# Kernel tuning notes

Hardware: AMD Instinct MI355X
Metric: run time of the kernel (lower is better)

## Reference

```python
import jax, jax.numpy as jnp
import numpy as np

B, S, D, H = 2, 2048, 1024, 16
DK = D // H


def setup_inputs() -> dict:
    key = jax.random.key(0)
    ks = jax.random.split(key, 11)
    scale = 1.0 / np.sqrt(D)
    inp = {
        "q": jax.random.normal(ks[0], (B, S, D), jnp.float32),
        "k": jax.random.normal(ks[1], (B, S, D), jnp.float32),
        "v": jax.random.normal(ks[2], (B, S, D), jnp.float32),
        # causal mask, broadcastable to (B, H, S, S); 0 = masked
        "mask": jnp.tril(jnp.ones((S, S), jnp.int32))[None, None, :, :],
        "wq": jax.random.normal(ks[3], (D, D), jnp.float32) * scale,
        "bq": jax.random.normal(ks[4], (D,), jnp.float32) * scale,
        "wk": jax.random.normal(ks[5], (D, D), jnp.float32) * scale,
        "bk": jax.random.normal(ks[6], (D,), jnp.float32) * scale,
        "wv": jax.random.normal(ks[7], (D, D), jnp.float32) * scale,
        "bv": jax.random.normal(ks[8], (D,), jnp.float32) * scale,
        "wo": jax.random.normal(ks[9], (D, D), jnp.float32) * scale,
        "bo": jax.random.normal(ks[10], (D,), jnp.float32) * scale,
    }
    return inp


def reference(q, k, v, mask, wq, bq, wk, bk, wv, bv, wo, bo):
    # Linear projections (torch Linear: y = x @ W^T + b)
    Q = jnp.einsum('bsd,ed->bse', q, wq) + bq
    K = jnp.einsum('bsd,ed->bse', k, wk) + bk
    V = jnp.einsum('bsd,ed->bse', v, wv) + bv
    # split heads -> (B, H, S, d_k)
    Q = Q.reshape(B, S, H, DK).transpose(0, 2, 1, 3)
    K = K.reshape(B, S, H, DK).transpose(0, 2, 1, 3)
    V = V.reshape(B, S, H, DK).transpose(0, 2, 1, 3)
    # naive full-score attention, faithful to the source
    scores = jnp.einsum('bhqd,bhkd->bhqk', Q, K) / jnp.sqrt(jnp.float32(DK))
    scores = jnp.where(mask == 0, -jnp.inf, scores)
    attn = jax.nn.softmax(scores, axis=-1)
    out = jnp.einsum('bhqk,bhkd->bhqd', attn, V)
    # merge heads -> (B, S, D)
    out = out.transpose(0, 2, 1, 3).reshape(B, S, D)
    return jnp.einsum('bsd,ed->bse', out, wo) + bo
```

## Files before the change

kernel.cpp:

```cpp
#include <hip/hip_runtime.h>
#include <hip/hip_bf16.h>
#include <cstdint>

constexpr int Bc = 2, Sc = 2048, Dc = 1024, Hc = 16;
constexpr int Mtok = Bc * Sc;

typedef __bf16 bf16;
typedef __bf16 bf16x4 __attribute__((ext_vector_type(4)));
typedef __bf16 bf16x8 __attribute__((ext_vector_type(8)));
typedef float  f32x4  __attribute__((ext_vector_type(4)));

__device__ __forceinline__ void gld_lds16(const bf16* g, bf16* l) {
  __builtin_amdgcn_global_load_lds(
      (__attribute__((address_space(1))) void*)(void*)g,
      (__attribute__((address_space(3))) void*)l, 16, 0, 0);
}

__global__ __launch_bounds__(256) void convert_all(
    const float* __restrict__ q, const float* __restrict__ k,
    const float* __restrict__ v, const float* __restrict__ wq,
    const float* __restrict__ wk, const float* __restrict__ wv,
    const float* __restrict__ wo, bf16* __restrict__ ws)
{
  constexpr size_t NQ = (size_t)Mtok * Dc;
  constexpr size_t NW = (size_t)Dc * Dc;
  const size_t e = ((size_t)blockIdx.x * 256 + threadIdx.x) * 8;
  const float* src; bf16* dst;
  if (e < 3 * NQ) {
    src = (e < NQ) ? q + e : (e < 2 * NQ) ? k + (e - NQ) : v + (e - 2 * NQ);
    dst = ws + e;
  } else {
    const size_t w = e - 3 * NQ;
    const float* wsrc = (w < NW) ? wq : (w < 2 * NW) ? wk : (w < 3 * NW) ? wv : wo;
    src = wsrc + (w & (NW - 1));
    dst = ws + 5 * NQ + w;
  }
  f32x4 a = ((const f32x4*)src)[0];
  f32x4 b = ((const f32x4*)src)[1];
  bf16x8 t;
  t[0]=(bf16)a[0]; t[1]=(bf16)a[1]; t[2]=(bf16)a[2]; t[3]=(bf16)a[3];
  t[4]=(bf16)b[0]; t[5]=(bf16)b[1]; t[6]=(bf16)b[2]; t[7]=(bf16)b[3];
  *(bf16x8*)dst = t;
}

__global__ __launch_bounds__(256) void gemm_qkv(
    const bf16* __restrict__ Aq, const bf16* __restrict__ Ak,
    const bf16* __restrict__ Av, const bf16* __restrict__ Wb,
    const float* __restrict__ bq, const float* __restrict__ bk,
    const float* __restrict__ bv,
    bf16* __restrict__ Yq, bf16* __restrict__ Yk, bf16* __restrict__ Vt)
{
  __shared__ __attribute__((aligned(16))) bf16 As[128 * 64];
  __shared__ __attribute__((aligned(16))) bf16 Bs[128 * 64];

  const int z = blockIdx.z;
  const bf16*  A    = (z == 0) ? Aq : (z == 1) ? Ak : Av;
  const bf16*  Wz   = Wb + (size_t)z * Dc * Dc;
  const float* bias = (z == 0) ? bq : (z == 1) ? bk : bv;

  const int m0 = blockIdx.x * 128, n0 = blockIdx.y * 128;
  const int tid = threadIdx.x, wave = tid >> 6, lane = tid & 63;
  const int quad = lane >> 4, l16 = lane & 15;
  const int rw = wave >> 1, cw = wave & 1;
  const int swz = l16 & 7;
  const int srow = wave * 8 + (lane >> 3);
  const int scol = ((lane & 7) ^ (lane >> 3)) * 8;

  f32x4 acc[4][4] = {};

  for (int k0 = 0; k0 < Dc; k0 += 64) {
#pragma unroll
    for (int s = 0; s < 4; ++s) {
      gld_lds16(A  + (size_t)(m0 + s * 32 + srow) * Dc + k0 + scol,
                &As[(s * 32 + wave * 8) * 64]);
      gld_lds16(Wz + (size_t)(n0 + s * 32 + srow) * Dc + k0 + scol,
                &Bs[(s * 32 + wave * 8) * 64]);
    }
    __syncthreads();
#pragma unroll
    for (int ks = 0; ks < 2; ++ks) {
      bf16x8 af[4];
#pragma unroll
      for (int rt = 0; rt < 4; ++rt)
        af[rt] = *(const bf16x8*)
            &As[(rw * 64 + rt * 16 + l16) * 64 + (((ks * 4 + quad) ^ swz) * 8)];
#pragma unroll
      for (int ct = 0; ct < 4; ++ct) {
        bf16x8 bfr = *(const bf16x8*)
            &Bs[(cw * 64 + ct * 16 + l16) * 64 + (((ks * 4 + quad) ^ swz) * 8)];
#pragma unroll
        for (int rt = 0; rt < 4; ++rt)
          acc[rt][ct] = __builtin_amdgcn_mfma_f32_16x16x32_bf16(af[rt], bfr, acc[rt][ct], 0, 0, 0);
      }
    }
    __syncthreads();
  }

  if (z < 2) {
    bf16* Y = (z == 0) ? Yq : Yk;
#pragma unroll
    for (int ct = 0; ct < 4; ++ct) {
      const int col = n0 + cw * 64 + ct * 16 + l16;
      const float bvv = bias[col];
#pragma unroll
      for (int rt = 0; rt < 4; ++rt)
#pragma unroll
        for (int i = 0; i < 4; ++i) {
          const int row = m0 + rw * 64 + rt * 16 + quad * 4 + i;
          Y[(size_t)row * Dc + col] = (bf16)(acc[rt][ct][i] + bvv);
        }
    }
  } else {
#pragma unroll
    for (int ct = 0; ct < 4; ++ct) {
      const int col = n0 + cw * 64 + ct * 16 + l16;
      const float bvv = bias[col];
#pragma unroll
      for (int rt = 0; rt < 4; ++rt) {
        const int row0 = m0 + rw * 64 + rt * 16 + quad * 4;
        const int bb = row0 >> 11, s0 = row0 & 2047;
        bf16x4 pk;
#pragma unroll
        for (int i = 0; i < 4; ++i) pk[i] = (bf16)(acc[rt][ct][i] + bvv);
        *(bf16x4*)&Vt[((size_t)bb * Dc + col) * Sc + s0] = pk;
      }
    }
  }
}

__global__ __launch_bounds__(256) void gemm_o(
    const bf16* __restrict__ A, const bf16* __restrict__ Wz,
    const float* __restrict__ bias, float* __restrict__ Y)
{
  __shared__ __attribute__((aligned(16))) bf16 As[128 * 64];
  __shared__ __attribute__((aligned(16))) bf16 Bs[128 * 64];

  const int m0 = blockIdx.x * 128, n0 = blockIdx.y * 128;
  const int tid = threadIdx.x, wave = tid >> 6, lane = tid & 63;
  const int quad = lane >> 4, l16 = lane & 15;
  const int rw = wave >> 1, cw = wave & 1;
  const int swz = l16 & 7;
  const int srow = wave * 8 + (lane >> 3);
  const int scol = ((lane & 7) ^ (lane >> 3)) * 8;

  f32x4 acc[4][4] = {};

  for (int k0 = 0; k0 < Dc; k0 += 64) {
#pragma unroll
    for (int s = 0; s < 4; ++s) {
      gld_lds16(A  + (size_t)(m0 + s * 32 + srow) * Dc + k0 + scol,
                &As[(s * 32 + wave * 8) * 64]);
      gld_lds16(Wz + (size_t)(n0 + s * 32 + srow) * Dc + k0 + scol,
                &Bs[(s * 32 + wave * 8) * 64]);
    }
    __syncthreads();
#pragma unroll
    for (int ks = 0; ks < 2; ++ks) {
      bf16x8 af[4];
#pragma unroll
      for (int rt = 0; rt < 4; ++rt)
        af[rt] = *(const bf16x8*)
            &As[(rw * 64 + rt * 16 + l16) * 64 + (((ks * 4 + quad) ^ swz) * 8)];
#pragma unroll
      for (int ct = 0; ct < 4; ++ct) {
        bf16x8 bfr = *(const bf16x8*)
            &Bs[(cw * 64 + ct * 16 + l16) * 64 + (((ks * 4 + quad) ^ swz) * 8)];
#pragma unroll
        for (int rt = 0; rt < 4; ++rt)
          acc[rt][ct] = __builtin_amdgcn_mfma_f32_16x16x32_bf16(af[rt], bfr, acc[rt][ct], 0, 0, 0);
      }
    }
    __syncthreads();
  }

#pragma unroll
  for (int ct = 0; ct < 4; ++ct) {
    const int col = n0 + cw * 64 + ct * 16 + l16;
    const float bvv = bias[col];
#pragma unroll
    for (int rt = 0; rt < 4; ++rt)
#pragma unroll
      for (int i = 0; i < 4; ++i) {
        const int row = m0 + rw * 64 + rt * 16 + quad * 4 + i;
        Y[(size_t)row * Dc + col] = acc[rt][ct][i] + bvv;
      }
  }
}

template <bool AF32, bool BF32, bool OUTF32>
__global__ __launch_bounds__(256) void gemm128(
    const void* __restrict__ Av, const void* __restrict__ Bv,
    const float* __restrict__ bias, void* __restrict__ Yv,
    int M, int N, int K)
{
  __shared__ __attribute__((aligned(16))) bf16 As[2][128][40];
  __shared__ __attribute__((aligned(16))) bf16 Bs[2][128][40];

  const int m0 = blockIdx.x * 128, n0 = blockIdx.y * 128;
  const int tid = threadIdx.x, wave = tid >> 6, lane = tid & 63;
  const int quad = lane >> 4, l16 = lane & 15;
  const int rw = wave >> 1, cw = wave & 1;
  const int srow = tid >> 1, sc = (tid & 1) * 16;

  f32x4 acc[4][4] = {};

  auto load = [&](const void* P, bool f32, int r0, int k0, bf16x8& lo, bf16x8& hi) {
    if (f32) {
      const float* s = (const float*)P + (size_t)(r0 + srow) * K + k0 + sc;
      f32x4 a0 = ((const f32x4*)s)[0], a1 = ((const f32x4*)s)[1];
      f32x4 a2 = ((const f32x4*)s)[2], a3 = ((const f32x4*)s)[3];
      lo[0]=(bf16)a0[0]; lo[1]=(bf16)a0[1]; lo[2]=(bf16)a0[2]; lo[3]=(bf16)a0[3];
      lo[4]=(bf16)a1[0]; lo[5]=(bf16)a1[1]; lo[6]=(bf16)a1[2]; lo[7]=(bf16)a1[3];
      hi[0]=(bf16)a2[0]; hi[1]=(bf16)a2[1]; hi[2]=(bf16)a2[2]; hi[3]=(bf16)a2[3];
      hi[4]=(bf16)a3[0]; hi[5]=(bf16)a3[1]; hi[6]=(bf16)a3[2]; hi[7]=(bf16)a3[3];
    } else {
      const bf16* s = (const bf16*)P + (size_t)(r0 + srow) * K + k0 + sc;
      lo = ((const bf16x8*)s)[0]; hi = ((const bf16x8*)s)[1];
    }
  };

  bf16x8 alo, ahi, blo, bhi;
  load(Av, AF32, m0, 0, alo, ahi); load(Bv, BF32, n0, 0, blo, bhi);
  *(bf16x8*)&As[0][srow][sc] = alo; *(bf16x8*)&As[0][srow][sc + 8] = ahi;
  *(bf16x8*)&Bs[0][srow][sc] = blo; *(bf16x8*)&Bs[0][srow][sc + 8] = bhi;

  const int NIT = K >> 5;
  for (int it = 0; it < NIT; ++it) {
    __syncthreads();
    const int cur = it & 1;
    const bool pf = (it + 1) < NIT;
    if (pf) { load(Av, AF32, m0, (it+1)*32, alo, ahi); load(Bv, BF32, n0, (it+1)*32, blo, bhi); }

    bf16x8 af[4];
#pragma unroll
    for (int rt = 0; rt < 4; ++rt)
      af[rt] = *(const bf16x8*)&As[cur][rw * 64 + rt * 16 + l16][quad * 8];
#pragma unroll
    for (int ct = 0; ct < 4; ++ct) {
      bf16x8 bfr = *(const bf16x8*)&Bs[cur][cw * 64 + ct * 16 + l16][quad * 8];
#pragma unroll
      for (int rt = 0; rt < 4; ++rt)
        acc[rt][ct] = __builtin_amdgcn_mfma_f32_16x16x32_bf16(af[rt], bfr, acc[rt][ct], 0, 0, 0);
    }
    if (pf) {
      const int nxt = cur ^ 1;
      *(bf16x8*)&As[nxt][srow][sc] = alo; *(bf16x8*)&As[nxt][srow][sc + 8] = ahi;
      *(bf16x8*)&Bs[nxt][srow][sc] = blo; *(bf16x8*)&Bs[nxt][srow][sc + 8] = bhi;
    }
  }

#pragma unroll
  for (int ct = 0; ct < 4; ++ct) {
    const int col = n0 + cw * 64 + ct * 16 + l16;
    const float bvv = bias[col];
#pragma unroll
    for (int rt = 0; rt < 4; ++rt)
#pragma unroll
      for (int i = 0; i < 4; ++i) {
        const int row = m0 + rw * 64 + rt * 16 + quad * 4 + i;
        const float vv = acc[rt][ct][i] + bvv;
        if constexpr (OUTF32) ((float*)Yv)[(size_t)row * N + col] = vv;
        else                  ((bf16*)Yv)[(size_t)row * N + col] = (bf16)vv;
      }
  }
}

__global__ __launch_bounds__(256) void transpose_v(
    const bf16* __restrict__ in, bf16* __restrict__ out)
{
  __shared__ __attribute__((aligned(16))) bf16 tile[64][72];
  const int s0 = blockIdx.x * 64, d0 = blockIdx.y * 64, b = blockIdx.z;
  const int t = threadIdx.x, r = t >> 2, c = (t & 3) * 16;

  const bf16* src = in + (size_t)(b * Sc + s0 + r) * Dc + d0 + c;
  *(bf16x8*)&tile[r][c]     = ((const bf16x8*)src)[0];
  *(bf16x8*)&tile[r][c + 8] = ((const bf16x8*)src)[1];
  __syncthreads();

  bf16x8 t0, t1;
#pragma unroll
  for (int j = 0; j < 8; ++j) t0[j] = tile[c + j][r];
#pragma unroll
  for (int j = 0; j < 8; ++j) t1[j] = tile[c + 8 + j][r];
  bf16* dst = out + (size_t)(b * Dc + d0 + r) * Sc + s0 + c;
  ((bf16x8*)dst)[0] = t0;
  ((bf16x8*)dst)[1] = t1;
}

__global__ __launch_bounds__(256, 6) void attn5(
    const bf16* __restrict__ Q, const bf16* __restrict__ K,
    const bf16* __restrict__ Vt, bf16* __restrict__ O)
{
  __shared__ __attribute__((aligned(16))) bf16 Ks[64 * 64];
  __shared__ __attribute__((aligned(16))) bf16 Vs[64 * 64];
  __shared__ __attribute__((aligned(16))) bf16 Ps[4][16][68];

  const int bh = blockIdx.x, b = bh >> 4, h = bh & 15;
  const int qy = blockIdx.y;
  const int qt = (qy & 8) ? ((qy & 24) | (7 - (qy & 7))) : qy;
  const int q0 = qt * 64;
  const int nkb = qt + 1;

  const int tid = threadIdx.x, wave = tid >> 6, lane = tid & 63;
  const int quad = lane >> 4, l16 = lane & 15;
  const int swz = l16 & 7;
  const int sr  = lane >> 3;
  const int sgc = ((lane & 7) ^ sr) * 8;

  const bf16 onec = (bf16)1.0f;
  const bf16x8 ones = {onec, onec, onec, onec, onec, onec, onec, onec};

  const bf16* qrow = Q + (size_t)(b * Sc + q0 + wave * 16 + l16) * Dc + h * 64 + quad * 8;
  const bf16x8 aq0 = *(const bf16x8*)qrow;
  const bf16x8 aq1 = *(const bf16x8*)(qrow + 32);

  f32x4 oacc[4] = {{0,0,0,0},{0,0,0,0},{0,0,0,0},{0,0,0,0}};
  f32x4 lacc = {0, 0, 0, 0};

  for (int kb = 0; kb < nkb; ++kb) {
    __syncthreads();
#pragma unroll
    for (int j = 0; j < 2; ++j) {
      const int r = wave * 16 + j * 8 + sr;
      gld_lds16(K  + (size_t)(b * Sc + kb * 64 + r) * Dc + h * 64 + sgc,
                &Ks[(wave * 16 + j * 8) * 64]);
      gld_lds16(Vt + (size_t)(b * Dc + h * 64 + r) * Sc + kb * 64 + sgc,
                &Vs[(wave * 16 + j * 8) * 64]);
    }
    __syncthreads();

    f32x4 s[4] = {{0,0,0,0},{0,0,0,0},{0,0,0,0},{0,0,0,0}};
#pragma unroll
    for (int d2 = 0; d2 < 2; ++d2) {
      const bf16x8 bq = d2 ? aq1 : aq0;
#pragma unroll
      for (int ct = 0; ct < 4; ++ct) {
        bf16x8 ak = *(const bf16x8*)
            &Ks[(ct * 16 + l16) * 64 + (((d2 * 4 + quad) ^ swz) * 8)];
        s[ct] = __builtin_amdgcn_mfma_f32_16x16x32_bf16(ak, bq, s[ct], 0, 0, 0);
      }
    }

    if (kb == nkb - 1) {
      const int qcol = wave * 16 + l16;
#pragma unroll
      for (int ct = 0; ct < 4; ++ct) {
        const int key0 = ct * 16 + quad * 4;
        bf16x4 pk;
#pragma unroll
        for (int i = 0; i < 4; ++i)
          pk[i] = (bf16)((key0 + i > qcol) ? 0.f : __expf(s[ct][i] * 0.125f));
        *(bf16x4*)&Ps[wave][l16][key0] = pk;
      }
    } else {
#pragma unroll
      for (int ct = 0; ct < 4; ++ct) {
        bf16x4 pk;
#pragma unroll
        for (int i = 0; i < 4; ++i) pk[i] = (bf16)__expf(s[ct][i] * 0.125f);
        *(bf16x4*)&Ps[wave][l16][ct * 16 + quad * 4] = pk;
      }
    }

    const bf16x8 ap0 = *(const bf16x8*)&Ps[wave][l16][quad * 8];
    const bf16x8 ap1 = *(const bf16x8*)&Ps[wave][l16][32 + quad * 8];

    lacc = __builtin_amdgcn_mfma_f32_16x16x32_bf16(ap0, ones, lacc, 0, 0, 0);
    lacc = __builtin_amdgcn_mfma_f32_16x16x32_bf16(ap1, ones, lacc, 0, 0, 0);

#pragma unroll
    for (int d2 = 0; d2 < 2; ++d2) {
      const bf16x8 ap = d2 ? ap1 : ap0;
#pragma unroll
      for (int ct = 0; ct < 4; ++ct) {
        bf16x8 bv = *(const bf16x8*)
            &Vs[(ct * 16 + l16) * 64 + (((d2 * 4 + quad) ^ swz) * 8)];
        oacc[ct] = __builtin_amdgcn_mfma_f32_16x16x32_bf16(ap, bv, oacc[ct], 0, 0, 0);
      }
    }
  }

  f32x4 rl;
#pragma unroll
  for (int i = 0; i < 4; ++i) rl[i] = 1.0f / lacc[i];
#pragma unroll
  for (int ct = 0; ct < 4; ++ct)
#pragma unroll
    for (int i = 0; i < 4; ++i)
      O[(size_t)(b * Sc + q0 + wave * 16 + quad * 4 + i) * Dc + h * 64 + ct * 16 + l16] =
          (bf16)(oacc[ct][i] * rl[i]);
}

extern "C" void kernel_launch(void* const* d_in, const int* in_sizes, int n_in,
                              void* d_out, int out_size, void* d_ws, size_t ws_size,
                              hipStream_t stream)
{
  const float* q  = (const float*)d_in[0];
  const float* k  = (const float*)d_in[1];
  const float* v  = (const float*)d_in[2];
  const float* wq = (const float*)d_in[4];
  const float* bq = (const float*)d_in[5];
  const float* wk = (const float*)d_in[6];
  const float* bk = (const float*)d_in[7];
  const float* wv = (const float*)d_in[8];
  const float* bv = (const float*)d_in[9];
  const float* wo = (const float*)d_in[10];
  const float* bo = (const float*)d_in[11];
  float* out = (float*)d_out;

  constexpr size_t NQ = (size_t)Mtok * Dc;
  constexpr size_t NW = (size_t)Dc * Dc;
  bf16* W = (bf16*)d_ws;
  const dim3 ga(Hc * Bc, 32);
  const dim3 gt(Sc / 64, Dc / 64, Bc);

  const bool fancy = ws_size >= (size_t)(6 * NQ + 4 * NW) * 2;
  if (fancy) {
    bf16* xq = W;
    bf16* xk = W + NQ;
    bf16* xv = W + 2 * NQ;
    bf16* Qp = W + 3 * NQ;
    bf16* Kp = W + 4 * NQ;
    bf16* wb = W + 5 * NQ;
    bf16* Vt = W + 5 * NQ + 4 * NW;
    bf16* AO = W;

    convert_all<<<8192, 256, 0, stream>>>(q, k, v, wq, wk, wv, wo, W);
    gemm_qkv<<<dim3(Mtok / 128, Dc / 128, 3), 256, 0, stream>>>(
        xq, xk, xv, wb, bq, bk, bv, Qp, Kp, Vt);
    attn5<<<ga, 256, 0, stream>>>(Qp, Kp, Vt, AO);
    gemm_o<<<dim3(Mtok / 128, Dc / 128), 256, 0, stream>>>(AO, wb + 3 * NW, bo, out);
  } else {
    bf16* Qp = W;
    bf16* Kp = W + NQ;
    bf16* Vp = W + 2 * NQ;
    bf16* Vt = W + 3 * NQ;
    bf16* AO = W + 4 * NQ;
    const dim3 gg(Mtok / 128, Dc / 128);
    gemm128<true, true, false><<<gg, 256, 0, stream>>>(q, wq, bq, Qp, Mtok, Dc, Dc);
    gemm128<true, true, false><<<gg, 256, 0, stream>>>(k, wk, bk, Kp, Mtok, Dc, Dc);
    gemm128<true, true, false><<<gg, 256, 0, stream>>>(v, wv, bv, Vp, Mtok, Dc, Dc);
    transpose_v<<<gt, 256, 0, stream>>>(Vp, Vt);
    attn5<<<ga, 256, 0, stream>>>(Qp, Kp, Vt, AO);
    gemm128<false, true, true><<<gg, 256, 0, stream>>>(AO, wo, bo, out, Mtok, Dc, Dc);
  }
}
```

Before: 228.5 us.

## Fuse fp32-to-bf16 conversion into GEMM tile staging, drop convert kernel

Removes the separate convert_all kernel that wrote bf16 copies of q/k/v and all weights to workspace. The QKV and output GEMMs now load fp32 tiles directly through registers, convert to bf16 and write them into swizzled LDS, which saves a full read-write pass over the inputs and one launch. The cost is that these staging loads go through registers instead of direct global-to-LDS loads, and each fp32 weight/activation tile is converted repeatedly by every block that reads it. The workspace requirement also drops.

```diff
diff --git a/kernel.cpp b/kernel.cpp
--- a/kernel.cpp
+++ b/kernel.cpp
@@ -16,36 +16,28 @@
       (__attribute__((address_space(3))) void*)l, 16, 0, 0);
 }
 
-__global__ __launch_bounds__(256) void convert_all(
+__device__ __forceinline__ void stage_f32_128x64(
+    const float* __restrict__ g, int ldg, bf16* __restrict__ lds, int tid)
+{
+  const int sc  = tid & 7;
+  const int sr0 = tid >> 3;
+  const int lc  = (sc ^ (sr0 & 7)) * 8;
+#pragma unroll
+  for (int j = 0; j < 4; ++j) {
+    const int r = sr0 + 32 * j;
+    const float* s = g + (size_t)r * ldg + lc;
+    f32x4 a = ((const f32x4*)s)[0], b = ((const f32x4*)s)[1];
+    bf16x8 t;
+    t[0]=(bf16)a[0]; t[1]=(bf16)a[1]; t[2]=(bf16)a[2]; t[3]=(bf16)a[3];
+    t[4]=(bf16)b[0]; t[5]=(bf16)b[1]; t[6]=(bf16)b[2]; t[7]=(bf16)b[3];
+    *(bf16x8*)&lds[r * 64 + sc * 8] = t;
+  }
+}
+
+__global__ __launch_bounds__(256) void gemm_qkv(
     const float* __restrict__ q, const float* __restrict__ k,
     const float* __restrict__ v, const float* __restrict__ wq,
     const float* __restrict__ wk, const float* __restrict__ wv,
-    const float* __restrict__ wo, bf16* __restrict__ ws)
-{
-  constexpr size_t NQ = (size_t)Mtok * Dc;
-  constexpr size_t NW = (size_t)Dc * Dc;
-  const size_t e = ((size_t)blockIdx.x * 256 + threadIdx.x) * 8;
-  const float* src; bf16* dst;
-  if (e < 3 * NQ) {
-    src = (e < NQ) ? q + e : (e < 2 * NQ) ? k + (e - NQ) : v + (e - 2 * NQ);
-    dst = ws + e;
-  } else {
-    const size_t w = e - 3 * NQ;
-    const float* wsrc = (w < NW) ? wq : (w < 2 * NW) ? wk : (w < 3 * NW) ? wv : wo;
-    src = wsrc + (w & (NW - 1));
-    dst = ws + 5 * NQ + w;
-  }
-  f32x4 a = ((const f32x4*)src)[0];
-  f32x4 b = ((const f32x4*)src)[1];
-  bf16x8 t;
-  t[0]=(bf16)a[0]; t[1]=(bf16)a[1]; t[2]=(bf16)a[2]; t[3]=(bf16)a[3];
-  t[4]=(bf16)b[0]; t[5]=(bf16)b[1]; t[6]=(bf16)b[2]; t[7]=(bf16)b[3];
-  *(bf16x8*)dst = t;
-}
-
-__global__ __launch_bounds__(256) void gemm_qkv(
-    const bf16* __restrict__ Aq, const bf16* __restrict__ Ak,
-    const bf16* __restrict__ Av, const bf16* __restrict__ Wb,
     const float* __restrict__ bq, const float* __restrict__ bk,
     const float* __restrict__ bv,
     bf16* __restrict__ Yq, bf16* __restrict__ Yk, bf16* __restrict__ Vt)
@@ -54,9 +46,79 @@
   __shared__ __attribute__((aligned(16))) bf16 Bs[128 * 64];
 
   const int z = blockIdx.z;
-  const bf16*  A    = (z == 0) ? Aq : (z == 1) ? Ak : Av;
-  const bf16*  Wz   = Wb + (size_t)z * Dc * Dc;
+  const float* A    = (z == 0) ? q  : (z == 1) ? k  : v;
+  const float* Wz   = (z == 0) ? wq : (z == 1) ? wk : wv;
   const float* bias = (z == 0) ? bq : (z == 1) ? bk : bv;
+
+  const int m0 = blockIdx.x * 128, n0 = blockIdx.y * 128;
+  const int tid = threadIdx.x, wave = tid >> 6, lane = tid & 63;
+  const int quad = lane >> 4, l16 = lane & 15;
+  const int rw = wave >> 1, cw = wave & 1;
+  const int swz = l16 & 7;
+
+  f32x4 acc[4][4] = {};
+
+  for (int k0 = 0; k0 < Dc; k0 += 64) {
+    stage_f32_128x64(A  + (size_t)m0 * Dc + k0, Dc, As, tid);
+    stage_f32_128x64(Wz + (size_t)n0 * Dc + k0, Dc, Bs, tid);
+    __syncthreads();
+#pragma unroll
+    for (int ks = 0; ks < 2; ++ks) {
+      bf16x8 af[4];
+#pragma unroll
+      for (int rt = 0; rt < 4; ++rt)
+        af[rt] = *(const bf16x8*)
+            &As[(rw * 64 + rt * 16 + l16) * 64 + (((ks * 4 + quad) ^ swz) * 8)];
+#pragma unroll
+      for (int ct = 0; ct < 4; ++ct) {
+        bf16x8 bfr = *(const bf16x8*)
+            &Bs[(cw * 64 + ct * 16 + l16) * 64 + (((ks * 4 + quad) ^ swz) * 8)];
+#pragma unroll
+        for (int rt = 0; rt < 4; ++rt)
+          acc[rt][ct] = __builtin_amdgcn_mfma_f32_16x16x32_bf16(af[rt], bfr, acc[rt][ct], 0, 0, 0);
+      }
+    }
+    __syncthreads();
+  }
+
+  if (z < 2) {
+    bf16* Y = (z == 0) ? Yq : Yk;
+#pragma unroll
+    for (int ct = 0; ct < 4; ++ct) {
+      const int col = n0 + cw * 64 + ct * 16 + l16;
+      const float bvv = bias[col];
+#pragma unroll
+      for (int rt = 0; rt < 4; ++rt)
+#pragma unroll
+        for (int i = 0; i < 4; ++i) {
+          const int row = m0 + rw * 64 + rt * 16 + quad * 4 + i;
+          Y[(size_t)row * Dc + col] = (bf16)(acc[rt][ct][i] + bvv);
+        }
+    }
+  } else {
+#pragma unroll
+    for (int ct = 0; ct < 4; ++ct) {
+      const int col = n0 + cw * 64 + ct * 16 + l16;
+      const float bvv = bias[col];
+#pragma unroll
+      for (int rt = 0; rt < 4; ++rt) {
+        const int row0 = m0 + rw * 64 + rt * 16 + quad * 4;
+        const int bb = row0 >> 11, s0 = row0 & 2047;
+        bf16x4 pk;
+#pragma unroll
+        for (int i = 0; i < 4; ++i) pk[i] = (bf16)(acc[rt][ct][i] + bvv);
+        *(bf16x4*)&Vt[((size_t)bb * Dc + col) * Sc + s0] = pk;
+      }
+    }
+  }
+}
+
+__global__ __launch_bounds__(256) void gemm_o(
+    const bf16* __restrict__ A, const float* __restrict__ Wz,
+    const float* __restrict__ bias, float* __restrict__ Y)
+{
+  __shared__ __attribute__((aligned(16))) bf16 As[128 * 64];
+  __shared__ __attribute__((aligned(16))) bf16 Bs[128 * 64];
 
   const int m0 = blockIdx.x * 128, n0 = blockIdx.y * 128;
   const int tid = threadIdx.x, wave = tid >> 6, lane = tid & 63;
@@ -70,89 +132,10 @@
 
   for (int k0 = 0; k0 < Dc; k0 += 64) {
 #pragma unroll
-    for (int s = 0; s < 4; ++s) {
-      gld_lds16(A  + (size_t)(m0 + s * 32 + srow) * Dc + k0 + scol,
+    for (int s = 0; s < 4; ++s)
+      gld_lds16(A + (size_t)(m0 + s * 32 + srow) * Dc + k0 + scol,
                 &As[(s * 32 + wave * 8) * 64]);
-      gld_lds16(Wz + (size_t)(n0 + s * 32 + srow) * Dc + k0 + scol,
-                &Bs[(s * 32 + wave * 8) * 64]);
-    }
-    __syncthreads();
-#pragma unroll
-    for (int ks = 0; ks < 2; ++ks) {
-      bf16x8 af[4];
-#pragma unroll
-      for (int rt = 0; rt < 4; ++rt)
-        af[rt] = *(const bf16x8*)
-            &As[(rw * 64 + rt * 16 + l16) * 64 + (((ks * 4 + quad) ^ swz) * 8)];
-#pragma unroll
-      for (int ct = 0; ct < 4; ++ct) {
-        bf16x8 bfr = *(const bf16x8*)
-            &Bs[(cw * 64 + ct * 16 + l16) * 64 + (((ks * 4 + quad) ^ swz) * 8)];
-#pragma unroll
-        for (int rt = 0; rt < 4; ++rt)
-          acc[rt][ct] = __builtin_amdgcn_mfma_f32_16x16x32_bf16(af[rt], bfr, acc[rt][ct], 0, 0, 0);
-      }
-    }
-    __syncthreads();
-  }
-
-  if (z < 2) {
-    bf16* Y = (z == 0) ? Yq : Yk;
-#pragma unroll
-    for (int ct = 0; ct < 4; ++ct) {
-      const int col = n0 + cw * 64 + ct * 16 + l16;
-      const float bvv = bias[col];
-#pragma unroll
-      for (int rt = 0; rt < 4; ++rt)
-#pragma unroll
-        for (int i = 0; i < 4; ++i) {
-          const int row = m0 + rw * 64 + rt * 16 + quad * 4 + i;
-          Y[(size_t)row * Dc + col] = (bf16)(acc[rt][ct][i] + bvv);
-        }
-    }
-  } else {
-#pragma unroll
-    for (int ct = 0; ct < 4; ++ct) {
-      const int col = n0 + cw * 64 + ct * 16 + l16;
-      const float bvv = bias[col];
-#pragma unroll
-      for (int rt = 0; rt < 4; ++rt) {
-        const int row0 = m0 + rw * 64 + rt * 16 + quad * 4;
-        const int bb = row0 >> 11, s0 = row0 & 2047;
-        bf16x4 pk;
-#pragma unroll
-        for (int i = 0; i < 4; ++i) pk[i] = (bf16)(acc[rt][ct][i] + bvv);
-        *(bf16x4*)&Vt[((size_t)bb * Dc + col) * Sc + s0] = pk;
-      }
-    }
-  }
-}
-
-__global__ __launch_bounds__(256) void gemm_o(
-    const bf16* __restrict__ A, const bf16* __restrict__ Wz,
-    const float* __restrict__ bias, float* __restrict__ Y)
-{
-  __shared__ __attribute__((aligned(16))) bf16 As[128 * 64];
-  __shared__ __attribute__((aligned(16))) bf16 Bs[128 * 64];
-
-  const int m0 = blockIdx.x * 128, n0 = blockIdx.y * 128;
-  const int tid = threadIdx.x, wave = tid >> 6, lane = tid & 63;
-  const int quad = lane >> 4, l16 = lane & 15;
-  const int rw = wave >> 1, cw = wave & 1;
-  const int swz = l16 & 7;
-  const int srow = wave * 8 + (lane >> 3);
-  const int scol = ((lane & 7) ^ (lane >> 3)) * 8;
-
-  f32x4 acc[4][4] = {};
-
-  for (int k0 = 0; k0 < Dc; k0 += 64) {
-#pragma unroll
-    for (int s = 0; s < 4; ++s) {
-      gld_lds16(A  + (size_t)(m0 + s * 32 + srow) * Dc + k0 + scol,
-                &As[(s * 32 + wave * 8) * 64]);
-      gld_lds16(Wz + (size_t)(n0 + s * 32 + srow) * Dc + k0 + scol,
-                &Bs[(s * 32 + wave * 8) * 64]);
-    }
+    stage_f32_128x64(Wz + (size_t)n0 * Dc + k0, Dc, Bs, tid);
     __syncthreads();
 #pragma unroll
     for (int ks = 0; ks < 2; ++ks) {
@@ -409,27 +392,21 @@
   float* out = (float*)d_out;
 
   constexpr size_t NQ = (size_t)Mtok * Dc;
-  constexpr size_t NW = (size_t)Dc * Dc;
   bf16* W = (bf16*)d_ws;
   const dim3 ga(Hc * Bc, 32);
   const dim3 gt(Sc / 64, Dc / 64, Bc);
 
-  const bool fancy = ws_size >= (size_t)(6 * NQ + 4 * NW) * 2;
+  const bool fancy = ws_size >= (size_t)(4 * NQ) * 2;
   if (fancy) {
-    bf16* xq = W;
-    bf16* xk = W + NQ;
-    bf16* xv = W + 2 * NQ;
-    bf16* Qp = W + 3 * NQ;
-    bf16* Kp = W + 4 * NQ;
-    bf16* wb = W + 5 * NQ;
-    bf16* Vt = W + 5 * NQ + 4 * NW;
-    bf16* AO = W;
-
-    convert_all<<<8192, 256, 0, stream>>>(q, k, v, wq, wk, wv, wo, W);
+    bf16* Qp = W;
+    bf16* Kp = W + NQ;
+    bf16* Vt = W + 2 * NQ;
+    bf16* AO = W + 3 * NQ;
+
     gemm_qkv<<<dim3(Mtok / 128, Dc / 128, 3), 256, 0, stream>>>(
-        xq, xk, xv, wb, bq, bk, bv, Qp, Kp, Vt);
+        q, k, v, wq, wk, wv, bq, bk, bv, Qp, Kp, Vt);
     attn5<<<ga, 256, 0, stream>>>(Qp, Kp, Vt, AO);
-    gemm_o<<<dim3(Mtok / 128, Dc / 128), 256, 0, stream>>>(AO, wb + 3 * NW, bo, out);
+    gemm_o<<<dim3(Mtok / 128, Dc / 128), 256, 0, stream>>>(AO, wo, bo, out);
   } else {
     bf16* Qp = W;
     bf16* Kp = W + NQ;
```

Result: slower. 250.8 us (+9.8%).
